# Kernel tuning notes

Measured on AMD Instinct MI355X. Metric: run time of the kernel, lower is better.

The kernel has to match this reference:

```python
import jax, jax.numpy as jnp
import numpy as np

N, E, G = 50000, 600000, 256
IN_C, EMB, HID, OUT = 64, 128, 128, 36


def _glorot(key, fan_in, fan_out):
    lim = np.sqrt(6.0 / (fan_in + fan_out)).astype(np.float32)
    return jax.random.uniform(key, (fan_in, fan_out), jnp.float32, -lim, lim)


def setup_inputs() -> dict:
    key = jax.random.key(0)
    ks = jax.random.split(key, 12)
    x = jax.random.normal(ks[0], (N, IN_C), jnp.float32)
    edge_index = jax.random.randint(ks[1], (2, E), 0, N, jnp.int64)
    edge_attr = jax.random.uniform(ks[2], (E,), jnp.float32)
    # deterministic sorted batch assignment -> every graph id 0..G-1 is nonempty
    batch = ((jnp.arange(N, dtype=jnp.int64) * G) // N).astype(jnp.int64)
    rho = jax.random.uniform(ks[3], (G,), jnp.float32)
    return {
        "x": x,
        "edge_attr": edge_attr,
        "rho": rho,
        "conv0_w": _glorot(ks[4], IN_C, EMB),
        "conv0_b": jnp.zeros((EMB,), jnp.float32),
        "conv1_w": _glorot(ks[5], EMB, EMB),
        "conv1_b": jnp.zeros((EMB,), jnp.float32),
        "mlp0_w": _glorot(ks[6], 2 * EMB + 1, HID),
        "mlp0_b": jnp.zeros((HID,), jnp.float32),
        "mlp1_w": _glorot(ks[7], HID, HID),
        "mlp1_b": jnp.zeros((HID,), jnp.float32),
        "out_w": _glorot(ks[8], HID, OUT),
        "out_b": jnp.zeros((OUT,), jnp.float32),
        "edge_index": edge_index,
        "batch": batch,
    }


def _gcn_conv(h, row, col, w, W, b):
    # PyG GCNConv: self-loops already appended in (row, col, w).
    deg = jax.ops.segment_sum(w, col, num_segments=N)  # in-degree by edge weight
    dis = jnp.where(deg > 0, jax.lax.rsqrt(jnp.maximum(deg, 1e-30)), 0.0)
    norm = dis[row] * w * dis[col]                     # [E+N]
    h = h @ W                                          # [N, out]
    msg = norm[:, None] * h[row]                       # gather + scale
    return jax.ops.segment_sum(msg, col, num_segments=N) + b


def reference(x, edge_attr, rho, conv0_w, conv0_b, conv1_w, conv1_b,
              mlp0_w, mlp0_b, mlp1_w, mlp1_b, out_w, out_b,
              edge_index, batch):
    # add self-loops with weight 1
    loops = jnp.arange(N, dtype=edge_index.dtype)
    row = jnp.concatenate([edge_index[0], loops])
    col = jnp.concatenate([edge_index[1], loops])
    w = jnp.concatenate([edge_attr, jnp.ones((N,), edge_attr.dtype)])

    h = jax.nn.relu(_gcn_conv(x, row, col, w, conv0_w, conv0_b))
    h = jax.nn.relu(_gcn_conv(h, row, col, w, conv1_w, conv1_b))

    gmp = jax.ops.segment_max(h, batch, num_segments=G)             # [G, EMB]
    cnt = jax.ops.segment_sum(jnp.ones((N,), h.dtype), batch, num_segments=G)
    gap = jax.ops.segment_sum(h, batch, num_segments=G) / cnt[:, None]
    hg = jnp.concatenate([gmp, gap, rho[:, None]], axis=1)          # [G, 2*EMB+1]

    hg = jax.nn.relu(hg @ mlp0_w + mlp0_b)
    hg = jax.nn.relu(hg @ mlp1_w + mlp1_b)
    return hg @ out_w + out_b
```

## Files before the change

kernel.cpp:

```cpp
#include <hip/hip_runtime.h>
#include <hip/hip_fp16.h>
#include <math.h>

using half8 = __attribute__((ext_vector_type(8))) _Float16;
using f32x4 = __attribute__((ext_vector_type(4))) float;

#define CAP 48
#define NPBSH 8
#define REG 4096
#define BSTRIDE 16


__device__ __forceinline__ float wdec(unsigned int v) {
    __half h;
    *reinterpret_cast<unsigned short*>(&h) = (unsigned short)(v >> 16);
    return __half2float(h);
}

__device__ __forceinline__ unsigned int wenc(int src, float w) {
    __half h = __float2half(w);
    return (unsigned int)src |
           ((unsigned int)(*reinterpret_cast<unsigned short*>(&h)) << 16);
}

__device__ __forceinline__ float4 ld_half4(const __half* p) {
    int2 raw = *reinterpret_cast<const int2*>(p);
    __half2 a = *reinterpret_cast<__half2*>(&raw.x);
    __half2 b = *reinterpret_cast<__half2*>(&raw.y);
    return make_float4(__low2float(a), __high2float(a), __low2float(b), __high2float(b));
}

__device__ __forceinline__ void st_half4(__half* p, float4 v) {
    __half2 a = __floats2half2_rn(v.x, v.y);
    __half2 b = __floats2half2_rn(v.z, v.w);
    int2 raw;
    raw.x = *reinterpret_cast<int*>(&a);
    raw.y = *reinterpret_cast<int*>(&b);
    *reinterpret_cast<int2*>(p) = raw;
}


__global__ void k_setup(const float* __restrict__ w0, __half* __restrict__ wt0,
                        const float* __restrict__ w1, __half* __restrict__ wt1,
                        int* __restrict__ bcnt, float* __restrict__ pmax,
                        float* __restrict__ psum, int nbp, int gch) {
    int i = blockIdx.x * blockDim.x + threadIdx.x;
    if (i < 64 * 128) {
        int k = i >> 7, c = i & 127;
        wt0[c * 64 + k] = __float2half(w0[i]);
    }
    if (i < 128 * 128) {
        int k = i >> 7, c = i & 127;
        wt1[c * 128 + k] = __float2half(w1[i]);
    }
    if (i < nbp) bcnt[i] = 0;
    if (i < gch) { pmax[i] = 0.f; psum[i] = 0.f; }
}


__global__ __launch_bounds__(256) void k_partA(
    const int* __restrict__ row, const int* __restrict__ col,
    const float* __restrict__ w, int* __restrict__ bcnt,
    uint2* __restrict__ regn, int e, int nb)
{
    __shared__ int lcnt[256];
    __shared__ int lbase[256];
    const int tid = threadIdx.x;
    for (int b = tid; b < nb; b += 256) lcnt[b] = 0;
    __syncthreads();
    const int base = blockIdx.x * 2048;
    int myb[8], myrank[8];
#pragma unroll
    for (int k = 0; k < 8; ++k) {
        int i = base + k * 256 + tid;
        if (i < e) {
            int b = col[i] >> NPBSH;
            myb[k] = b;
            myrank[k] = atomicAdd(&lcnt[b], 1);
        } else myb[k] = -1;
    }
    __syncthreads();
    for (int b = tid; b < nb; b += 256) {
        int c = lcnt[b];
        lbase[b] = (c > 0) ? atomicAdd(&bcnt[b * BSTRIDE], c) : 0;
    }
    __syncthreads();
#pragma unroll
    for (int k = 0; k < 8; ++k) {
        int i = base + k * 256 + tid;
        if (myb[k] >= 0) {
            int pos = lbase[myb[k]] + myrank[k];
            if (pos < REG) {
                uint2 rec;
                rec.x = (unsigned)row[i] | (((unsigned)col[i] & 255u) << 16);
                rec.y = __float_as_uint(w[i]);
                regn[(size_t)myb[k] * REG + pos] = rec;
            }
        }
    }
}


__global__ __launch_bounds__(256) void k_partB(
    const uint2* __restrict__ regn, const int* __restrict__ bcnt,
    const float* __restrict__ x, unsigned int* __restrict__ slab,
    int* __restrict__ cnt_g, float* __restrict__ dis,
    __half* __restrict__ xs, int n)
{
    __shared__ unsigned int simg[256 * CAP];
    __shared__ int lcnt[256];
    __shared__ float lwsum[256];
    __shared__ float sdis[256];
    const int tid = threadIdx.x;
    const int b = blockIdx.x;
    lcnt[tid] = 0; lwsum[tid] = 0.f;
    __syncthreads();
    int ce = bcnt[b * BSTRIDE]; if (ce > REG) ce = REG;
    for (int i = tid; i < ce; i += 256) {
        uint2 rec = regn[(size_t)b * REG + i];
        int nl = (rec.x >> 16) & 255;
        int r = (int)(rec.x & 0xFFFFu);
        float w = __uint_as_float(rec.y);
        int s = atomicAdd(&lcnt[nl], 1);
        if (s < CAP) simg[nl * CAP + s] = wenc(r, w);
        atomicAdd(&lwsum[nl], w);
    }
    __syncthreads();
    const int node0 = b << NPBSH;
    int nodes_here = n - node0; if (nodes_here > 256) nodes_here = 256;
    if (nodes_here <= 0) return;
    if (tid < nodes_here) {
        int node = node0 + tid;
        int c = lcnt[tid]; if (c > CAP) c = CAP;
        cnt_g[node] = c;
        float d = rsqrtf(1.0f + lwsum[tid]);
        dis[node] = d;
        sdis[tid] = d;
    }
    __syncthreads();
    for (int idx = tid; idx < nodes_here * CAP; idx += 256)
        slab[(size_t)node0 * CAP + idx] = simg[idx];
    for (int q = tid; q < nodes_here * 16; q += 256) {
        int nl = q >> 4;
        float d = sdis[nl];
        float4 v = reinterpret_cast<const float4*>(x)[(size_t)node0 * 16 + q];
        v.x *= d; v.y *= d; v.z *= d; v.w *= d;
        st_half4(&xs[((size_t)node0 * 16 + q) * 4], v);
    }
}


template<int COLS, int LPN>
__global__ __launch_bounds__(256) void k_agg(
    const __half* __restrict__ hs, const unsigned int* __restrict__ slab,
    const int* __restrict__ cursor, const float* __restrict__ dis,
    __half* __restrict__ out, int n)
{
    int t = blockIdx.x * blockDim.x + threadIdx.x;
    int node = t / LPN, lane = t % LPN;
    if (node >= n) return;
    int c4 = lane * 4;
    float4 acc = ld_half4(&hs[(size_t)node * COLS + c4]);
    int cnt = min(cursor[node], CAP);
    const unsigned int* sp = &slab[(size_t)node * CAP];
    int p = 0;
    for (; p + 4 <= cnt; p += 4) {
        uint4 rec = *reinterpret_cast<const uint4*>(&sp[p]);
        float w0 = wdec(rec.x), w1 = wdec(rec.y), w2 = wdec(rec.z), w3 = wdec(rec.w);
        float4 v0 = ld_half4(&hs[(size_t)(rec.x & 0xFFFF) * COLS + c4]);
        float4 v1 = ld_half4(&hs[(size_t)(rec.y & 0xFFFF) * COLS + c4]);
        float4 v2 = ld_half4(&hs[(size_t)(rec.z & 0xFFFF) * COLS + c4]);
        float4 v3 = ld_half4(&hs[(size_t)(rec.w & 0xFFFF) * COLS + c4]);
        acc.x = fmaf(w0, v0.x, acc.x); acc.y = fmaf(w0, v0.y, acc.y);
        acc.z = fmaf(w0, v0.z, acc.z); acc.w = fmaf(w0, v0.w, acc.w);
        acc.x = fmaf(w1, v1.x, acc.x); acc.y = fmaf(w1, v1.y, acc.y);
        acc.z = fmaf(w1, v1.z, acc.z); acc.w = fmaf(w1, v1.w, acc.w);
        acc.x = fmaf(w2, v2.x, acc.x); acc.y = fmaf(w2, v2.y, acc.y);
        acc.z = fmaf(w2, v2.z, acc.z); acc.w = fmaf(w2, v2.w, acc.w);
        acc.x = fmaf(w3, v3.x, acc.x); acc.y = fmaf(w3, v3.y, acc.y);
        acc.z = fmaf(w3, v3.z, acc.z); acc.w = fmaf(w3, v3.w, acc.w);
    }
    for (; p < cnt; ++p) {
        unsigned int rec = sp[p];
        float w0 = wdec(rec);
        float4 v0 = ld_half4(&hs[(size_t)(rec & 0xFFFF) * COLS + c4]);
        acc.x = fmaf(w0, v0.x, acc.x); acc.y = fmaf(w0, v0.y, acc.y);
        acc.z = fmaf(w0, v0.z, acc.z); acc.w = fmaf(w0, v0.w, acc.w);
    }
    float d = dis[node];
    float4 o;
    o.x = d * acc.x; o.y = d * acc.y; o.z = d * acc.z; o.w = d * acc.w;
    st_half4(&out[(size_t)node * COLS + c4], o);
}


template<int K, bool SC, bool POOL>
__global__ __launch_bounds__(256) void k_gemm_mfma(
    const __half* __restrict__ A, const __half* __restrict__ wt,
    const float* __restrict__ bias, const float* __restrict__ scale,
    const int* __restrict__ batch, float* __restrict__ pmax,
    float* __restrict__ psum, __half* __restrict__ out, int n)
{
    constexpr int SA = K + 8;
    constexpr int CPR = K / 8;
    __shared__ _Float16 Al[64 * SA];
    __shared__ _Float16 Wl[128 * SA];
    const int tid = threadIdx.x;
    const int row0 = blockIdx.x * 64;

#pragma unroll
    for (int it = 0; it < (64 * CPR) / 256; ++it) {
        int id = tid + it * 256;
        int r = id / CPR, kc = id % CPR;
        int gr = row0 + r; if (gr >= n) gr = n - 1;
        int4 raw = *reinterpret_cast<const int4*>(&A[(size_t)gr * K + kc * 8]);
        *reinterpret_cast<int4*>(&Al[r * SA + kc * 8]) = raw;
    }
#pragma unroll
    for (int it = 0; it < (128 * CPR) / 256; ++it) {
        int id = tid + it * 256;
        int c = id / CPR, kc = id % CPR;
        int4 raw = *reinterpret_cast<const int4*>(&wt[(size_t)c * K + kc * 8]);
        *reinterpret_cast<int4*>(&Wl[c * SA + kc * 8]) = raw;
    }
    __syncthreads();

    const int l = tid & 63, w = tid >> 6;
    const int r = l & 15, kg = l >> 4;

    f32x4 acc[8];
#pragma unroll
    for (int ct = 0; ct < 8; ++ct) acc[ct] = (f32x4){0.f, 0.f, 0.f, 0.f};

#pragma unroll
    for (int kst = 0; kst < K / 32; ++kst) {
        half8 af = *reinterpret_cast<const half8*>(&Al[(16 * w + r) * SA + kst * 32 + kg * 8]);
#pragma unroll
        for (int ct = 0; ct < 8; ++ct) {
            half8 bf = *reinterpret_cast<const half8*>(&Wl[(16 * ct + r) * SA + kst * 32 + kg * 8]);
            acc[ct] = __builtin_amdgcn_mfma_f32_16x16x32_f16(af, bf, acc[ct], 0, 0, 0);
        }
    }

    float sc[4];
    int bq[4];
    int g0 = 0, g1 = 0;
    if constexpr (POOL) {
        g0 = batch[row0];
        g1 = batch[(row0 + 63 < n) ? row0 + 63 : n - 1];
    }
#pragma unroll
    for (int q = 0; q < 4; ++q) {
        int gr = row0 + 16 * w + kg * 4 + q;
        sc[q] = (SC && gr < n) ? scale[gr] : 1.0f;
        if constexpr (POOL) bq[q] = (gr < n) ? (batch[gr] - g0) : -1;
    }
    float pm0[8], ps0[8], pm1[8], ps1[8];
    if constexpr (POOL) {
#pragma unroll
        for (int ct = 0; ct < 8; ++ct) { pm0[ct] = 0.f; ps0[ct] = 0.f; pm1[ct] = 0.f; ps1[ct] = 0.f; }
    }
#pragma unroll
    for (int ct = 0; ct < 8; ++ct) {
        float bv = bias[16 * ct + r];
#pragma unroll
        for (int q = 0; q < 4; ++q) {
            int gr = row0 + 16 * w + kg * 4 + q;
            if (gr < n) {
                float v = fmaxf(acc[ct][q] + bv, 0.f);
                if constexpr (SC) v *= sc[q];
                out[(size_t)gr * 128 + 16 * ct + r] = __float2half(v);
                if constexpr (POOL) {
                    if (bq[q] == 0) { pm0[ct] = fmaxf(pm0[ct], v); ps0[ct] += v; }
                    else if (bq[q] == 1) { pm1[ct] = fmaxf(pm1[ct], v); ps1[ct] += v; }
                }
            }
        }
    }

    if constexpr (POOL) {
#pragma unroll
        for (int mask = 16; mask <= 32; mask <<= 1) {
#pragma unroll
            for (int ct = 0; ct < 8; ++ct) {
                pm0[ct] = fmaxf(pm0[ct], __shfl_xor(pm0[ct], mask));
                ps0[ct] += __shfl_xor(ps0[ct], mask);
                pm1[ct] = fmaxf(pm1[ct], __shfl_xor(pm1[ct], mask));
                ps1[ct] += __shfl_xor(ps1[ct], mask);
            }
        }
        __syncthreads();
        float* ldsm = reinterpret_cast<float*>(Wl);
        float* ldss = ldsm + 4 * 2 * 128;
        if (kg == 0) {
#pragma unroll
            for (int ct = 0; ct < 8; ++ct) {
                int ch = 16 * ct + r;
                ldsm[(w * 2 + 0) * 128 + ch] = pm0[ct];
                ldsm[(w * 2 + 1) * 128 + ch] = pm1[ct];
                ldss[(w * 2 + 0) * 128 + ch] = ps0[ct];
                ldss[(w * 2 + 1) * 128 + ch] = ps1[ct];
            }
        }
        __syncthreads();
        int gslot = tid >> 7, ch = tid & 127;
        bool valid = (gslot == 0) || (g1 != g0);
        if (valid) {
            float M = 0.f, S = 0.f;
#pragma unroll
            for (int ww = 0; ww < 4; ++ww) {
                M = fmaxf(M, ldsm[(ww * 2 + gslot) * 128 + ch]);
                S += ldss[(ww * 2 + gslot) * 128 + ch];
            }
            int g = g0 + gslot;
            atomicMax(reinterpret_cast<int*>(&pmax[(size_t)g * 128 + ch]), __float_as_int(M));
            atomicAdd(&psum[(size_t)g * 128 + ch], S);
        }
    }
}


__device__ __forceinline__ int lowbound(const int* __restrict__ b, int n, int key) {
    int lo = 0, hi = n;
    while (lo < hi) { int mid = (lo + hi) >> 1; if (b[mid] < key) lo = mid + 1; else hi = mid; }
    return lo;
}

__global__ __launch_bounds__(256) void k_head_mlp(
    const float* __restrict__ pmax, const float* __restrict__ psum,
    const int* __restrict__ batch, const float* __restrict__ rho,
    const float* __restrict__ w0, const float* __restrict__ b0,
    const float* __restrict__ w1, const float* __restrict__ b1,
    const float* __restrict__ w2, const float* __restrict__ b2,
    float* __restrict__ out, int n)
{
    int g = blockIdx.x;
    int tid = threadIdx.x;
    int ch = tid & 127, half = tid >> 7;
    __shared__ float hg[257];
    __shared__ float t0[128];
    __shared__ float red[2][128];
    __shared__ int scnt;
    if (tid == 0) {
        int beg = lowbound(batch, n, g);
        int end = lowbound(batch, n, g + 1);
        scnt = end - beg;
        hg[256] = rho[g];
    }
    __syncthreads();
    if (half == 0) {
        hg[ch] = pmax[(size_t)g * 128 + ch];
        hg[128 + ch] = psum[(size_t)g * 128 + ch] / (float)scnt;
    }
    __syncthreads();
    {
        float a = 0.f, b = 0.f;
        int j0 = half * 128;
        int jend = half ? 257 : 128;
        int j = j0;
        for (; j + 2 <= jend; j += 2) {
            a = fmaf(hg[j], w0[(size_t)j * 128 + ch], a);
            b = fmaf(hg[j + 1], w0[(size_t)(j + 1) * 128 + ch], b);
        }
        if (j < jend) a = fmaf(hg[j], w0[(size_t)j * 128 + ch], a);
        red[half][ch] = a + b;
        __syncthreads();
        if (half == 0) t0[ch] = fmaxf(red[0][ch] + red[1][ch] + b0[ch], 0.f);
        __syncthreads();
    }
    {
        float a = 0.f, b = 0.f;
        int j0 = half * 64;
        for (int j = j0; j < j0 + 64; j += 2) {
            a = fmaf(t0[j], w1[(size_t)j * 128 + ch], a);
            b = fmaf(t0[j + 1], w1[(size_t)(j + 1) * 128 + ch], b);
        }
        red[half][ch] = a + b;
        __syncthreads();
        if (half == 0) hg[ch] = fmaxf(red[0][ch] + red[1][ch] + b1[ch], 0.f);
        __syncthreads();
    }
    if (ch < 36) {
        float a = 0.f, b = 0.f;
        int j0 = half * 64;
        for (int j = j0; j < j0 + 64; j += 2) {
            a = fmaf(hg[j], w2[(size_t)j * 36 + ch], a);
            b = fmaf(hg[j + 1], w2[(size_t)(j + 1) * 36 + ch], b);
        }
        red[half][ch] = a + b;
    }
    __syncthreads();
    if (half == 0 && ch < 36)
        out[(size_t)g * 36 + ch] = red[0][ch] + red[1][ch] + b2[ch];
}


extern "C" void kernel_launch(void* const* d_in, const int* in_sizes, int n_in,
                              void* d_out, int out_size, void* d_ws, size_t ws_size,
                              hipStream_t stream)
{
    const float* x        = (const float*)d_in[0];
    const float* edge_attr= (const float*)d_in[1];
    const float* rho      = (const float*)d_in[2];
    const float* conv0_w  = (const float*)d_in[3];
    const float* conv0_b  = (const float*)d_in[4];
    const float* conv1_w  = (const float*)d_in[5];
    const float* conv1_b  = (const float*)d_in[6];
    const float* mlp0_w   = (const float*)d_in[7];
    const float* mlp0_b   = (const float*)d_in[8];
    const float* mlp1_w   = (const float*)d_in[9];
    const float* mlp1_b   = (const float*)d_in[10];
    const float* out_w    = (const float*)d_in[11];
    const float* out_b    = (const float*)d_in[12];
    const int*   edge_idx = (const int*)d_in[13];
    const int*   batch    = (const int*)d_in[14];

    const int N = in_sizes[0] / 64;
    const int E = in_sizes[1];
    const int G = in_sizes[2];
    const int* erow = edge_idx;
    const int* ecol = edge_idx + E;
    const int NB = (N + 255) >> NPBSH;

    char* ws = (char*)d_ws;
    size_t off = 0;
    auto alloc = [&](size_t bytes) -> void* {
        off = (off + 255) & ~(size_t)255;
        void* p = ws + off;
        off += bytes;
        return p;
    };
    float*        dis    = (float*)alloc((size_t)N * 4);
    int*          cnt_g  = (int*)  alloc((size_t)N * 4);
    int*          bcnt   = (int*)  alloc((size_t)NB * BSTRIDE * 4);
    uint2*        regn   = (uint2*)alloc((size_t)NB * REG * 8);
    unsigned int* slab   = (unsigned int*)alloc((size_t)N * CAP * 4);
    __half*       bufA   = (__half*)alloc((size_t)N * 128 * 2);
    __half*       bufB   = (__half*)alloc((size_t)N * 128 * 2);
    float*        pmax   = (float*)alloc((size_t)G * 128 * 4);
    float*        psum   = (float*)alloc((size_t)G * 128 * 4);
    __half*       wt0    = (__half*)alloc((size_t)64 * 128 * 2);
    __half*       wt1    = (__half*)alloc((size_t)128 * 128 * 2);

    dim3 b256(256);
    int gch = G * 128;
    int nbp = NB * BSTRIDE;
    int setup_n = 128 * 128;
    if (setup_n < nbp) setup_n = nbp;
    if (setup_n < gch) setup_n = gch;
    k_setup<<<(setup_n + 255) / 256, b256, 0, stream>>>(conv0_w, wt0, conv1_w, wt1,
                                                       bcnt, pmax, psum, nbp, gch);
    k_partA<<<(E + 2047) / 2048, b256, 0, stream>>>(erow, ecol, edge_attr, bcnt, regn, E, NB);
    k_partB<<<NB, b256, 0, stream>>>(regn, bcnt, x, slab, cnt_g, dis, bufA, N);

    k_agg<64, 16><<<((size_t)N * 16 + 255) / 256, b256, 0, stream>>>(bufA, slab, cnt_g, dis, bufB, N);
    k_gemm_mfma<64, true, false><<<(N + 63) / 64, b256, 0, stream>>>(
        bufB, wt0, conv0_b, dis, nullptr, nullptr, nullptr, bufA, N);
    k_agg<128, 32><<<((size_t)N * 32 + 255) / 256, b256, 0, stream>>>(bufA, slab, cnt_g, dis, bufB, N);
    k_gemm_mfma<128, false, true><<<(N + 63) / 64, b256, 0, stream>>>(
        bufB, wt1, conv1_b, nullptr, batch, pmax, psum, bufA, N);

    k_head_mlp<<<G, b256, 0, stream>>>(pmax, psum, batch, rho,
                                       mlp0_w, mlp0_b, mlp1_w, mlp1_b, out_w, out_b,
                                       (float*)d_out, N);
}
```

Measured before the change: 144.1 us.

## Halve partition bucket size, widen aggregation loads, fold setup into partB

Several changes at once. Bucket size drops from 256 to 128 nodes, doubling the number of partB blocks. The weight transpose moves into partB and the setup kernel becomes a memset of a contiguous zeroed region. The aggregation kernel now uses 8-wide half loads with half the lanes per node. Each node's neighbour list is insertion-sorted and the degree is summed serially, replacing a shared float atomic, which makes the sums deterministic and may improve gather locality but adds per-thread serial work.

```diff
diff --git a/kernel.cpp b/kernel.cpp
--- a/kernel.cpp
+++ b/kernel.cpp
@@ -6,8 +6,8 @@
 using f32x4 = __attribute__((ext_vector_type(4))) float;
 
 #define CAP 48
-#define NPBSH 8
-#define REG 4096
+#define NPBSH 7
+#define REG 2048
 #define BSTRIDE 16
 
 
@@ -21,13 +21,6 @@
     __half h = __float2half(w);
     return (unsigned int)src |
            ((unsigned int)(*reinterpret_cast<unsigned short*>(&h)) << 16);
-}
-
-__device__ __forceinline__ float4 ld_half4(const __half* p) {
-    int2 raw = *reinterpret_cast<const int2*>(p);
-    __half2 a = *reinterpret_cast<__half2*>(&raw.x);
-    __half2 b = *reinterpret_cast<__half2*>(&raw.y);
-    return make_float4(__low2float(a), __high2float(a), __low2float(b), __high2float(b));
 }
 
 __device__ __forceinline__ void st_half4(__half* p, float4 v) {
@@ -40,31 +33,13 @@
 }
 
 
-__global__ void k_setup(const float* __restrict__ w0, __half* __restrict__ wt0,
-                        const float* __restrict__ w1, __half* __restrict__ wt1,
-                        int* __restrict__ bcnt, float* __restrict__ pmax,
-                        float* __restrict__ psum, int nbp, int gch) {
-    int i = blockIdx.x * blockDim.x + threadIdx.x;
-    if (i < 64 * 128) {
-        int k = i >> 7, c = i & 127;
-        wt0[c * 64 + k] = __float2half(w0[i]);
-    }
-    if (i < 128 * 128) {
-        int k = i >> 7, c = i & 127;
-        wt1[c * 128 + k] = __float2half(w1[i]);
-    }
-    if (i < nbp) bcnt[i] = 0;
-    if (i < gch) { pmax[i] = 0.f; psum[i] = 0.f; }
-}
-
-
 __global__ __launch_bounds__(256) void k_partA(
     const int* __restrict__ row, const int* __restrict__ col,
     const float* __restrict__ w, int* __restrict__ bcnt,
     uint2* __restrict__ regn, int e, int nb)
 {
-    __shared__ int lcnt[256];
-    __shared__ int lbase[256];
+    __shared__ int lcnt[512];
+    __shared__ int lbase[512];
     const int tid = threadIdx.x;
     for (int b = tid; b < nb; b += 256) lcnt[b] = 0;
     __syncthreads();
@@ -92,7 +67,7 @@
             int pos = lbase[myb[k]] + myrank[k];
             if (pos < REG) {
                 uint2 rec;
-                rec.x = (unsigned)row[i] | (((unsigned)col[i] & 255u) << 16);
+                rec.x = (unsigned)row[i] | (((unsigned)col[i] & 127u) << 16);
                 rec.y = __float_as_uint(w[i]);
                 regn[(size_t)myb[k] * REG + pos] = rec;
             }
@@ -104,37 +79,57 @@
 __global__ __launch_bounds__(256) void k_partB(
     const uint2* __restrict__ regn, const int* __restrict__ bcnt,
     const float* __restrict__ x, unsigned int* __restrict__ slab,
-    int* __restrict__ cnt_g, float* __restrict__ dis,
-    __half* __restrict__ xs, int n)
-{
-    __shared__ unsigned int simg[256 * CAP];
-    __shared__ int lcnt[256];
-    __shared__ float lwsum[256];
-    __shared__ float sdis[256];
+    int* __restrict__ cnt_g, float* __restrict__ dis, __half* __restrict__ xs,
+    const float* __restrict__ w0, __half* __restrict__ wt0,
+    const float* __restrict__ w1, __half* __restrict__ wt1, int n)
+{
+    __shared__ unsigned int simg[128 * CAP];
+    __shared__ int lcnt[128];
+    __shared__ float sdis[128];
     const int tid = threadIdx.x;
     const int b = blockIdx.x;
-    lcnt[tid] = 0; lwsum[tid] = 0.f;
+
+    {
+        int wi = b * 256 + tid;
+        if (wi < 64 * 128) {
+            int k = wi >> 7, c = wi & 127;
+            wt0[c * 64 + k] = __float2half(w0[wi]);
+        } else if (wi < 64 * 128 + 128 * 128) {
+            int i2 = wi - 64 * 128;
+            int k = i2 >> 7, c = i2 & 127;
+            wt1[c * 128 + k] = __float2half(w1[i2]);
+        }
+    }
+
+    if (tid < 128) lcnt[tid] = 0;
     __syncthreads();
     int ce = bcnt[b * BSTRIDE]; if (ce > REG) ce = REG;
     for (int i = tid; i < ce; i += 256) {
         uint2 rec = regn[(size_t)b * REG + i];
-        int nl = (rec.x >> 16) & 255;
+        int nl = (rec.x >> 16) & 127;
         int r = (int)(rec.x & 0xFFFFu);
         float w = __uint_as_float(rec.y);
         int s = atomicAdd(&lcnt[nl], 1);
         if (s < CAP) simg[nl * CAP + s] = wenc(r, w);
-        atomicAdd(&lwsum[nl], w);
     }
     __syncthreads();
     const int node0 = b << NPBSH;
-    int nodes_here = n - node0; if (nodes_here > 256) nodes_here = 256;
+    int nodes_here = n - node0; if (nodes_here > 128) nodes_here = 128;
     if (nodes_here <= 0) return;
     if (tid < nodes_here) {
-        int node = node0 + tid;
         int c = lcnt[tid]; if (c > CAP) c = CAP;
-        cnt_g[node] = c;
-        float d = rsqrtf(1.0f + lwsum[tid]);
-        dis[node] = d;
+        cnt_g[node0 + tid] = c;
+        unsigned int* L = &simg[tid * CAP];
+        for (int a = 1; a < c; ++a) {
+            unsigned int key = L[a];
+            int q = a - 1;
+            while (q >= 0 && L[q] > key) { L[q + 1] = L[q]; --q; }
+            L[q + 1] = key;
+        }
+        float s = 1.0f;
+        for (int j = 0; j < c; ++j) s += wdec(L[j]);
+        float d = rsqrtf(s);
+        dis[node0 + tid] = d;
         sdis[tid] = d;
     }
     __syncthreads();
@@ -159,38 +154,43 @@
     int t = blockIdx.x * blockDim.x + threadIdx.x;
     int node = t / LPN, lane = t % LPN;
     if (node >= n) return;
-    int c4 = lane * 4;
-    float4 acc = ld_half4(&hs[(size_t)node * COLS + c4]);
+    int c8 = lane * 8;
+    float acc[8];
+    {
+        half8 v = *reinterpret_cast<const half8*>(&hs[(size_t)node * COLS + c8]);
+#pragma unroll
+        for (int u = 0; u < 8; ++u) acc[u] = (float)v[u];
+    }
     int cnt = min(cursor[node], CAP);
     const unsigned int* sp = &slab[(size_t)node * CAP];
     int p = 0;
     for (; p + 4 <= cnt; p += 4) {
         uint4 rec = *reinterpret_cast<const uint4*>(&sp[p]);
         float w0 = wdec(rec.x), w1 = wdec(rec.y), w2 = wdec(rec.z), w3 = wdec(rec.w);
-        float4 v0 = ld_half4(&hs[(size_t)(rec.x & 0xFFFF) * COLS + c4]);
-        float4 v1 = ld_half4(&hs[(size_t)(rec.y & 0xFFFF) * COLS + c4]);
-        float4 v2 = ld_half4(&hs[(size_t)(rec.z & 0xFFFF) * COLS + c4]);
-        float4 v3 = ld_half4(&hs[(size_t)(rec.w & 0xFFFF) * COLS + c4]);
-        acc.x = fmaf(w0, v0.x, acc.x); acc.y = fmaf(w0, v0.y, acc.y);
-        acc.z = fmaf(w0, v0.z, acc.z); acc.w = fmaf(w0, v0.w, acc.w);
-        acc.x = fmaf(w1, v1.x, acc.x); acc.y = fmaf(w1, v1.y, acc.y);
-        acc.z = fmaf(w1, v1.z, acc.z); acc.w = fmaf(w1, v1.w, acc.w);
-        acc.x = fmaf(w2, v2.x, acc.x); acc.y = fmaf(w2, v2.y, acc.y);
-        acc.z = fmaf(w2, v2.z, acc.z); acc.w = fmaf(w2, v2.w, acc.w);
-        acc.x = fmaf(w3, v3.x, acc.x); acc.y = fmaf(w3, v3.y, acc.y);
-        acc.z = fmaf(w3, v3.z, acc.z); acc.w = fmaf(w3, v3.w, acc.w);
+        half8 v0 = *reinterpret_cast<const half8*>(&hs[(size_t)(rec.x & 0xFFFF) * COLS + c8]);
+        half8 v1 = *reinterpret_cast<const half8*>(&hs[(size_t)(rec.y & 0xFFFF) * COLS + c8]);
+        half8 v2 = *reinterpret_cast<const half8*>(&hs[(size_t)(rec.z & 0xFFFF) * COLS + c8]);
+        half8 v3 = *reinterpret_cast<const half8*>(&hs[(size_t)(rec.w & 0xFFFF) * COLS + c8]);
+#pragma unroll
+        for (int u = 0; u < 8; ++u) {
+            acc[u] = fmaf(w0, (float)v0[u], acc[u]);
+            acc[u] = fmaf(w1, (float)v1[u], acc[u]);
+            acc[u] = fmaf(w2, (float)v2[u], acc[u]);
+            acc[u] = fmaf(w3, (float)v3[u], acc[u]);
+        }
     }
     for (; p < cnt; ++p) {
         unsigned int rec = sp[p];
         float w0 = wdec(rec);
-        float4 v0 = ld_half4(&hs[(size_t)(rec & 0xFFFF) * COLS + c4]);
-        acc.x = fmaf(w0, v0.x, acc.x); acc.y = fmaf(w0, v0.y, acc.y);
-        acc.z = fmaf(w0, v0.z, acc.z); acc.w = fmaf(w0, v0.w, acc.w);
+        half8 v0 = *reinterpret_cast<const half8*>(&hs[(size_t)(rec & 0xFFFF) * COLS + c8]);
+#pragma unroll
+        for (int u = 0; u < 8; ++u) acc[u] = fmaf(w0, (float)v0[u], acc[u]);
     }
     float d = dis[node];
-    float4 o;
-    o.x = d * acc.x; o.y = d * acc.y; o.z = d * acc.z; o.w = d * acc.w;
-    st_half4(&out[(size_t)node * COLS + c4], o);
+    half8 o;
+#pragma unroll
+    for (int u = 0; u < 8; ++u) o[u] = (_Float16)(d * acc[u]);
+    *reinterpret_cast<half8*>(&out[(size_t)node * COLS + c8]) = o;
 }
 
 
@@ -420,7 +420,7 @@
     const int G = in_sizes[2];
     const int* erow = edge_idx;
     const int* ecol = edge_idx + E;
-    const int NB = (N + 255) >> NPBSH;
+    const int NB = (N + 127) >> NPBSH;
 
     char* ws = (char*)d_ws;
     size_t off = 0;
@@ -433,30 +433,27 @@
     float*        dis    = (float*)alloc((size_t)N * 4);
     int*          cnt_g  = (int*)  alloc((size_t)N * 4);
     int*          bcnt   = (int*)  alloc((size_t)NB * BSTRIDE * 4);
+    float*        pmax   = (float*)alloc((size_t)G * 128 * 4);
+    float*        psum   = (float*)alloc((size_t)G * 128 * 4);
+    size_t zend = off;
+    size_t zbeg = (size_t)((char*)bcnt - ws);
     uint2*        regn   = (uint2*)alloc((size_t)NB * REG * 8);
     unsigned int* slab   = (unsigned int*)alloc((size_t)N * CAP * 4);
     __half*       bufA   = (__half*)alloc((size_t)N * 128 * 2);
     __half*       bufB   = (__half*)alloc((size_t)N * 128 * 2);
-    float*        pmax   = (float*)alloc((size_t)G * 128 * 4);
-    float*        psum   = (float*)alloc((size_t)G * 128 * 4);
     __half*       wt0    = (__half*)alloc((size_t)64 * 128 * 2);
     __half*       wt1    = (__half*)alloc((size_t)128 * 128 * 2);
 
     dim3 b256(256);
-    int gch = G * 128;
-    int nbp = NB * BSTRIDE;
-    int setup_n = 128 * 128;
-    if (setup_n < nbp) setup_n = nbp;
-    if (setup_n < gch) setup_n = gch;
-    k_setup<<<(setup_n + 255) / 256, b256, 0, stream>>>(conv0_w, wt0, conv1_w, wt1,
-                                                       bcnt, pmax, psum, nbp, gch);
+    hipMemsetAsync(ws + zbeg, 0, zend - zbeg, stream);
     k_partA<<<(E + 2047) / 2048, b256, 0, stream>>>(erow, ecol, edge_attr, bcnt, regn, E, NB);
-    k_partB<<<NB, b256, 0, stream>>>(regn, bcnt, x, slab, cnt_g, dis, bufA, N);
-
-    k_agg<64, 16><<<((size_t)N * 16 + 255) / 256, b256, 0, stream>>>(bufA, slab, cnt_g, dis, bufB, N);
+    k_partB<<<NB, b256, 0, stream>>>(regn, bcnt, x, slab, cnt_g, dis, bufA,
+                                     conv0_w, wt0, conv1_w, wt1, N);
+
+    k_agg<64, 8><<<((size_t)N * 8 + 255) / 256, b256, 0, stream>>>(bufA, slab, cnt_g, dis, bufB, N);
     k_gemm_mfma<64, true, false><<<(N + 63) / 64, b256, 0, stream>>>(
         bufB, wt0, conv0_b, dis, nullptr, nullptr, nullptr, bufA, N);
-    k_agg<128, 32><<<((size_t)N * 32 + 255) / 256, b256, 0, stream>>>(bufA, slab, cnt_g, dis, bufB, N);
+    k_agg<128, 16><<<((size_t)N * 16 + 255) / 256, b256, 0, stream>>>(bufA, slab, cnt_g, dis, bufB, N);
     k_gemm_mfma<128, false, true><<<(N + 63) / 64, b256, 0, stream>>>(
         bufB, wt1, conv1_b, nullptr, batch, pmax, psum, bufA, N);
 
```

Measured after the change: 164.1 us. +13.8%, slower.
